# Kernel tuning notes

Measured on AMD Instinct MI355X. Metric: run time of the kernel, lower is better.

Reference implementation:

```python
import jax, jax.numpy as jnp
import numpy as np

N = 50000       # nodes
E = 1600000     # edges (avg degree 32)
IN = 128        # node_in_dim
D = 64          # node_out_dim (= GRU hidden)
H = 1           # heads
ED = 3          # edge_in_dim
STEPS = 3       # num_step_message_passing
EPS = 1e-5      # BatchNorm eps
SLOPE = 0.2     # LeakyReLU negative slope (GAT default)


def setup_inputs() -> dict:
    key = jax.random.key(0)
    ks = jax.random.split(key, 16)
    s_in = 1.0 / np.sqrt(IN)
    s_d = 1.0 / np.sqrt(D)
    return {
        "x": jax.random.normal(ks[0], (N, IN), jnp.float32),
        "edge_attr": jax.random.normal(ks[1], (E, ED), jnp.float32),
        "mlp_w": jax.random.normal(ks[2], (IN, D), jnp.float32) * s_in,
        "mlp_b": jnp.zeros((D,), jnp.float32),
        "bn_g": jnp.ones((D,), jnp.float32),
        "bn_b": jnp.zeros((D,), jnp.float32),
        "conv_w": jax.random.normal(ks[3], (D, H * D), jnp.float32) * s_d,
        "att_dst": jax.random.normal(ks[4], (H, D), jnp.float32) * s_d,
        "att_src": jax.random.normal(ks[5], (H, D), jnp.float32) * s_d,
        "att_edge": jax.random.normal(ks[6], (H, ED), jnp.float32) * s_d,
        "w_ih": jax.random.normal(ks[7], (3 * D, H * D), jnp.float32) * s_d,
        "w_hh": jax.random.normal(ks[8], (3 * D, D), jnp.float32) * s_d,
        "b_ih": jnp.zeros((3 * D,), jnp.float32),
        "b_hh": jnp.zeros((3 * D,), jnp.float32),
        "lin_w": jax.random.normal(ks[9], (IN, D), jnp.float32) * s_in,
        "lin_b": jnp.zeros((D,), jnp.float32),
        "edge_index": jax.random.randint(ks[10], (2, E), 0, N, jnp.int64),
    }


def _egat_conv(out, edge_attr, src, dst, conv_w, att_dst, att_src, att_edge):
    # out: [N, D] -> xt: [N, H, D]
    xt = (out @ conv_w).reshape(N, H, D)
    # per-node attention halves (avoid gathering twice): [N, H]
    a_dst_n = jnp.einsum("nhd,hd->nh", xt, att_dst)
    a_src_n = jnp.einsum("nhd,hd->nh", xt, att_src)
    # per-edge logits: [E, H]
    logits = a_dst_n[dst] + a_src_n[src] + edge_attr @ att_edge.T
    logits = jnp.where(logits >= 0, logits, SLOPE * logits)
    # segment softmax over destination nodes
    seg_max = jax.ops.segment_max(logits, dst, num_segments=N)  # [N, H]
    seg_max = jnp.where(jnp.isfinite(seg_max), seg_max, 0.0)
    expd = jnp.exp(logits - seg_max[dst])
    denom = jax.ops.segment_sum(expd, dst, num_segments=N)      # [N, H]
    alpha = expd / denom[dst]                                   # [E, H]
    # attention-weighted aggregation of source features
    msgs = alpha[:, :, None] * xt[src]                          # [E, H, D]
    agg = jax.ops.segment_sum(msgs, dst, num_segments=N)        # [N, H, D]
    return agg.reshape(N, H * D)


def _gru_cell(x_in, h, w_ih, w_hh, b_ih, b_hh):
    gi = x_in @ w_ih.T + b_ih
    gh = h @ w_hh.T + b_hh
    gi_r, gi_z, gi_n = jnp.split(gi, 3, axis=-1)
    gh_r, gh_z, gh_n = jnp.split(gh, 3, axis=-1)
    r = jax.nn.sigmoid(gi_r + gh_r)
    z = jax.nn.sigmoid(gi_z + gh_z)
    n = jnp.tanh(gi_n + r * gh_n)
    return (1.0 - z) * n + z * h


def reference(x, edge_attr, mlp_w, mlp_b, bn_g, bn_b, conv_w, att_dst,
              att_src, att_edge, w_ih, w_hh, b_ih, b_hh, lin_w, lin_b,
              edge_index):
    src, dst = edge_index[0], edge_index[1]
    # initial embedding: ReLU(BatchNorm(Linear(x))) with batch stats
    h0 = x @ mlp_w + mlp_b
    mu = jnp.mean(h0, axis=0)
    var = jnp.var(h0, axis=0)
    out = jax.nn.relu((h0 - mu) * jax.lax.rsqrt(var + EPS) * bn_g + bn_b)
    h = out
    for _ in range(STEPS):
        m = jax.nn.relu(_egat_conv(out, edge_attr, src, dst,
                                   conv_w, att_dst, att_src, att_edge))
        h = _gru_cell(m, h, w_ih, w_hh, b_ih, b_hh)
        out = h
    return x @ lin_w + lin_b + out
```

## Files before the change

kernel.cpp:

```cpp
#include <hip/hip_runtime.h>

typedef unsigned short ushort_t;
typedef unsigned int uint_t;
typedef __attribute__((ext_vector_type(8))) short bf16x8;
typedef __attribute__((ext_vector_type(4))) float f32x4;

#define N_NODES 50000
#define N_EDGES 1600000
#define NB_BKT 391
#define CAP_BKT 4608
#define CAP_B 6144

__device__ __forceinline__ float bfu(ushort_t u) {
    return __uint_as_float(((uint_t)u) << 16);
}
__device__ __forceinline__ ushort_t f2b(float f) {
    uint_t x = __float_as_uint(f);
    uint_t r = (x + 0x7FFFu + ((x >> 16) & 1u)) >> 16;
    return (ushort_t)r;
}
__device__ __forceinline__ float sigm(float x) {
    return 1.0f / (1.0f + __expf(-x));
}
__device__ __forceinline__ float tanh_f(float x) {
    return 1.0f - 2.0f / (__expf(2.0f * x) + 1.0f);
}
__device__ __forceinline__ bf16x8 pack8(const float* v) {
    bf16x8 r;
#pragma unroll
    for (int j = 0; j < 8; ++j) r[j] = (short)f2b(v[j]);
    return r;
}
__device__ __forceinline__ int ld_src(const int* __restrict__ ei, int i, int f64) {
    return f64 ? ei[2 * i] : ei[i];
}
__device__ __forceinline__ int ld_dst(const int* __restrict__ ei, int i, int f64) {
    return f64 ? ei[2 * N_EDGES + 2 * i] : ei[N_EDGES + i];
}
__device__ __forceinline__ bool is_f64(const int* flag) { return flag[0] > 2048; }

__global__ void k_sentinel(float* __restrict__ out, int n) {
    int i = blockIdx.x * 256 + threadIdx.x;
    if (i < n) out[i] = 100.0f;
}

__global__ void k_prep(const float* __restrict__ w_ih, const float* __restrict__ w_hh,
                       const float* __restrict__ conv_w, const float* __restrict__ mlp_w,
                       const float* __restrict__ lin_w, const int* __restrict__ ei,
                       ushort_t* __restrict__ wb, ushort_t* __restrict__ cwb,
                       ushort_t* __restrict__ mlpT, ushort_t* __restrict__ linT,
                       int* __restrict__ flag, int* __restrict__ gtail) {
    int blk = blockIdx.x;
    if (blk < 176) {
        int t = blk * 256 + threadIdx.x;
        if (t < 24576) {
            const float* w = (t < 12288) ? w_ih : w_hh;
            wb[t] = f2b(w[t < 12288 ? t : t - 12288]);
        } else if (t < 28672) {
            int r = t - 24576;
            int j = r >> 6, k = r & 63;
            cwb[j * 64 + k] = f2b(conv_w[k * 64 + j]);
        } else if (t < 36864) {
            int r = t - 28672;
            int j = r >> 7, k = r & 127;
            mlpT[j * 128 + k] = f2b(mlp_w[k * 64 + j]);
        } else if (t < 45056) {
            int r = t - 36864;
            int j = r >> 7, k = r & 127;
            linT[j * 128 + k] = f2b(lin_w[k * 64 + j]);
        }
    } else if (blk == 176) {
        __shared__ int red[256];
        int tid = threadIdx.x;
        int zeros = 0;
#pragma unroll
        for (int j = 0; j < 16; ++j) {
            int slot = (tid * 16 + j) * 2 + 1;
            if (ei[slot] == 0) zeros++;
        }
        red[tid] = zeros;
        __syncthreads();
        for (int off = 128; off; off >>= 1) {
            if (tid < off) red[tid] += red[tid + off];
            __syncthreads();
        }
        if (tid == 0) flag[0] = red[0];
    } else {
        int b = (blk - 177) * 256 + threadIdx.x;
        if (b < NB_BKT) gtail[b] = b * CAP_BKT;
    }
}

__global__ __launch_bounds__(256) void k_emb(const float* __restrict__ x,
                                             const ushort_t* __restrict__ mlpT,
                                             const float* __restrict__ mlp_b,
                                             float* __restrict__ h0, int n) {
    int lane = threadIdx.x & 63;
    int wv = threadIdx.x >> 6;
    int tile = blockIdx.x * 4 + wv;
    if (tile * 16 >= n) return;
    int nb16 = tile * 16;
    int mrow = lane & 15, q = lane >> 4;
    const float* xp = x + (nb16 + mrow) * 128 + q * 8;
    bf16x8 a[4];
#pragma unroll
    for (int kc = 0; kc < 4; ++kc) {
        float hv[8];
        const float* p = xp + kc * 32;
#pragma unroll
        for (int j = 0; j < 8; ++j) hv[j] = p[j];
        a[kc] = pack8(hv);
    }
    f32x4 acc[4];
#pragma unroll
    for (int t = 0; t < 4; ++t) acc[t] = (f32x4){0.f, 0.f, 0.f, 0.f};
#pragma unroll
    for (int kc = 0; kc < 4; ++kc) {
#pragma unroll
        for (int t = 0; t < 4; ++t) {
            bf16x8 b = *(const bf16x8*)(mlpT + (t * 16 + mrow) * 128 + kc * 32 + q * 8);
            acc[t] = __builtin_amdgcn_mfma_f32_16x16x32_bf16(a[kc], b, acc[t], 0, 0, 0);
        }
    }
#pragma unroll
    for (int t = 0; t < 4; ++t) {
        int j = t * 16 + mrow;
        float bias = mlp_b[j];
#pragma unroll
        for (int r = 0; r < 4; ++r) h0[(nb16 + q * 4 + r) * 64 + j] = acc[t][r] + bias;
    }
}

__global__ void k_stats(const float* __restrict__ h0, float* __restrict__ stats, int n) {
    __shared__ float ssum[256], ssq[256];
    int tid = threadIdx.x;
    int gid = blockIdx.x * 256 + tid;
    int col = gid & 63;
    int rg = gid >> 6;
    float s = 0.f, s2 = 0.f;
    for (int row = rg; row < n; row += 1024) {
        float v = h0[row * 64 + col];
        s += v;
        s2 += v * v;
    }
    ssum[tid] = s;
    ssq[tid] = s2;
    __syncthreads();
    if (tid < 64) {
        s = ssum[tid] + ssum[tid + 64] + ssum[tid + 128] + ssum[tid + 192];
        s2 = ssq[tid] + ssq[tid + 64] + ssq[tid + 128] + ssq[tid + 192];
        atomicAdd(&stats[tid], s);
        atomicAdd(&stats[64 + tid], s2);
    }
}

__global__ void k_bnrelu(const float* __restrict__ h0, const float* __restrict__ stats,
                         const float* __restrict__ g, const float* __restrict__ bb,
                         float* __restrict__ h, int total, float inv_n) {
    int i = blockIdx.x * 256 + threadIdx.x;
    if (i >= total) return;
    int j = i & 63;
    float mu = stats[j] * inv_n;
    float var = fmaxf(stats[64 + j] * inv_n - mu * mu, 0.f);
    float sc = rsqrtf(var + 1e-5f) * g[j];
    float sh = bb[j] - mu * sc;
    h[i] = fmaxf(h0[i] * sc + sh, 0.f);
}

__global__ __launch_bounds__(256) void k_bucket(const int* __restrict__ ei,
                                                const int* __restrict__ flag,
                                                const float* __restrict__ ea,
                                                const float* __restrict__ ae,
                                                int* __restrict__ gtail,
                                                uint2* __restrict__ bkt, int e) {
    __shared__ int cnt[NB_BKT];
    __shared__ int gbase[NB_BKT];
    for (int i = threadIdx.x; i < NB_BKT; i += 256) cnt[i] = 0;
    __syncthreads();
    int base = blockIdx.x * 4096;
    int f64 = is_f64(flag);
    float a0 = ae[0], a1 = ae[1], a2 = ae[2];
    uint_t w0[16];
    uint_t w1[16];
    int bk[16], rk[16];
#pragma unroll
    for (int j = 0; j < 16; ++j) {
        int i = base + j * 256 + threadIdx.x;
        bk[j] = -1;
        if (i < e) {
            int d = ld_dst(ei, i, f64);
            if ((uint_t)d < (uint_t)N_NODES) {
                int s = ld_src(ei, i, f64);
                if ((uint_t)s >= (uint_t)N_NODES) s = 0;
                float ed = ea[i * 3] * a0 + ea[i * 3 + 1] * a1 + ea[i * 3 + 2] * a2;
                bk[j] = d >> 7;
                w0[j] = (uint_t)s | ((uint_t)(d & 127) << 16);
                w1[j] = __float_as_uint(ed);
                rk[j] = atomicAdd(&cnt[bk[j]], 1);
            }
        }
    }
    __syncthreads();
    for (int t = threadIdx.x; t < NB_BKT; t += 256) {
        int c = cnt[t];
        gbase[t] = c ? atomicAdd(&gtail[t], c) : 0;
    }
    __syncthreads();
#pragma unroll
    for (int j = 0; j < 16; ++j) {
        if (bk[j] >= 0) {
            int pos = gbase[bk[j]] + rk[j];
            if (pos < (bk[j] + 1) * CAP_BKT) {
                uint2 p;
                p.x = w0[j];
                p.y = w1[j];
                bkt[pos] = p;
            }
        }
    }
}

__global__ __launch_bounds__(256) void k_sortb(const int* __restrict__ gtail,
                                               const uint2* __restrict__ bkt,
                                               uint2* __restrict__ pk,
                                               int* __restrict__ rs, int n) {
    __shared__ uint2 stg[CAP_B];
    __shared__ int cnt[128];
    __shared__ int sc[128];
    __shared__ int red[256];
    int b = blockIdx.x;
    int tid = threadIdx.x;
    int partial = 0;
    for (int i = tid; i < b; i += 256) partial += min(gtail[i] - i * CAP_BKT, CAP_BKT);
    red[tid] = partial;
    __syncthreads();
    for (int off = 128; off; off >>= 1) {
        if (tid < off) red[tid] += red[tid + off];
        __syncthreads();
    }
    int obase = red[0];
    int node0 = b * 128;
    int nloc = min(128, n - node0);
    int size = min(gtail[b] - b * CAP_BKT, CAP_BKT);
    const uint2* bin = bkt + b * CAP_BKT;
    for (int i = tid; i < 128; i += 256) cnt[i] = 0;
    __syncthreads();
    for (int ofs = tid; ofs < size; ofs += 256) {
        int dlow = (bin[ofs].x >> 16) & 127;
        atomicAdd(&cnt[dlow], 1);
    }
    __syncthreads();
    if (tid < 128) sc[tid] = cnt[tid];
    __syncthreads();
    for (int off = 1; off < 128; off <<= 1) {
        int add = (tid < 128 && tid >= off) ? sc[tid - off] : 0;
        __syncthreads();
        if (tid < 128) sc[tid] += add;
        __syncthreads();
    }
    if (tid < 128) sc[tid] -= cnt[tid];
    __syncthreads();
    if (tid < nloc) rs[node0 + tid] = obase + sc[tid];
    if (b == NB_BKT - 1 && tid == 0) rs[n] = obase + size;
    for (int i = tid; i < 128; i += 256) cnt[i] = 0;
    __syncthreads();
    for (int ofs = tid; ofs < size; ofs += 256) {
        uint2 p = bin[ofs];
        int dlow = (p.x >> 16) & 127;
        int r = atomicAdd(&cnt[dlow], 1);
        int pos = sc[dlow] + r;
        uint2 q;
        q.x = p.x & 0xFFFFu;
        q.y = p.y;
        if (pos < CAP_B) stg[pos] = q;
        else pk[obase + pos] = q;
    }
    __syncthreads();
    int wlim = min(size, CAP_B);
    for (int ofs = tid; ofs < wlim; ofs += 256) pk[obase + ofs] = stg[ofs];
}

__global__ __launch_bounds__(256) void k_xt(const float* __restrict__ h,
                                            const ushort_t* __restrict__ cwb,
                                            const float* __restrict__ att_dst,
                                            const float* __restrict__ att_src,
                                            ushort_t* __restrict__ xt,
                                            float* __restrict__ adst,
                                            float* __restrict__ asrc, int n) {
    int lane = threadIdx.x & 63;
    int wv = threadIdx.x >> 6;
    int tile = blockIdx.x * 4 + wv;
    if (tile * 16 >= n) return;
    int nb16 = tile * 16;
    int mrow = lane & 15, q = lane >> 4;
    bf16x8 ah[2];
    {
        const float* hp = h + (nb16 + mrow) * 64 + q * 8;
        float hv[8];
#pragma unroll
        for (int j = 0; j < 8; ++j) hv[j] = hp[j];
        ah[0] = pack8(hv);
#pragma unroll
        for (int j = 0; j < 8; ++j) hv[j] = hp[32 + j];
        ah[1] = pack8(hv);
    }
    f32x4 acc[4];
#pragma unroll
    for (int t = 0; t < 4; ++t) acc[t] = (f32x4){0.f, 0.f, 0.f, 0.f};
#pragma unroll
    for (int kh = 0; kh < 2; ++kh) {
#pragma unroll
        for (int t = 0; t < 4; ++t) {
            bf16x8 b = *(const bf16x8*)(cwb + (t * 16 + mrow) * 64 + kh * 32 + q * 8);
            acc[t] = __builtin_amdgcn_mfma_f32_16x16x32_bf16(ah[kh], b, acc[t], 0, 0, 0);
        }
    }
    float sd[4] = {0, 0, 0, 0}, ss[4] = {0, 0, 0, 0};
#pragma unroll
    for (int t = 0; t < 4; ++t) {
        int j = t * 16 + mrow;
        float ad = att_dst[j], as = att_src[j];
#pragma unroll
        for (int r = 0; r < 4; ++r) {
            float v = acc[t][r];
            xt[(nb16 + q * 4 + r) * 64 + j] = f2b(v);
            sd[r] += v * ad;
            ss[r] += v * as;
        }
    }
#pragma unroll
    for (int off = 1; off < 16; off <<= 1) {
#pragma unroll
        for (int r = 0; r < 4; ++r) {
            sd[r] += __shfl_xor(sd[r], off);
            ss[r] += __shfl_xor(ss[r], off);
        }
    }
    if (mrow == 0) {
#pragma unroll
        for (int r = 0; r < 4; ++r) {
            adst[nb16 + q * 4 + r] = sd[r];
            asrc[nb16 + q * 4 + r] = ss[r];
        }
    }
}

__global__ __launch_bounds__(256) void k_agg(const int* __restrict__ rs,
                                             const uint2* __restrict__ pk,
                                             const float* __restrict__ adst,
                                             const float* __restrict__ asrc,
                                             const ushort_t* __restrict__ xt,
                                             ushort_t* __restrict__ m, int n) {
    __shared__ float s_w[4][64];
    __shared__ int s_s[4][64];
    int lane = threadIdx.x & 63;
    int wv = threadIdx.x >> 6;
    int v = blockIdx.x * 4 + wv;
    if (v >= n) return;
    int start = rs[v], end = rs[v + 1];
    if (start >= end) {
        m[v * 64 + lane] = 0;
        return;
    }
    float adv = adst[v];
    int g = lane >> 3;
    int cb = (lane & 7) * 8;
    float acc[8] = {0, 0, 0, 0, 0, 0, 0, 0};
    float dsum = 0.f;
    for (int base = start; base < end; base += 64) {
        int e = base + lane;
        float w = 0.f;
        int s = 0;
        if (e < end) {
            uint2 p = pk[e];
            s = (int)p.x;
            float l = adv + asrc[s] + __uint_as_float(p.y);
            l = (l >= 0.f) ? l : 0.2f * l;
            w = __expf(l);
        }
        dsum += w;
        s_w[wv][lane] = w;
        s_s[wv][lane] = s;
        int cnt = min(64, end - base);
        int nb8 = (cnt + 7) >> 3;
        for (int tb = 0; tb < nb8; ++tb) {
            int sl = tb * 8 + g;
            float w8 = s_w[wv][sl];
            int s8 = s_s[wv][sl];
            uint4 qv = *(const uint4*)(xt + s8 * 64 + cb);
            acc[0] += w8 * __uint_as_float(qv.x << 16);
            acc[1] += w8 * __uint_as_float(qv.x & 0xFFFF0000u);
            acc[2] += w8 * __uint_as_float(qv.y << 16);
            acc[3] += w8 * __uint_as_float(qv.y & 0xFFFF0000u);
            acc[4] += w8 * __uint_as_float(qv.z << 16);
            acc[5] += w8 * __uint_as_float(qv.z & 0xFFFF0000u);
            acc[6] += w8 * __uint_as_float(qv.w << 16);
            acc[7] += w8 * __uint_as_float(qv.w & 0xFFFF0000u);
        }
    }
#pragma unroll
    for (int off = 32; off; off >>= 1) dsum += __shfl_xor(dsum, off);
#pragma unroll
    for (int off = 8; off < 64; off <<= 1) {
#pragma unroll
        for (int j = 0; j < 8; ++j) acc[j] += __shfl_xor(acc[j], off);
    }
    float inv = 1.0f / fmaxf(dsum, 1e-20f);
    if (g == 0) {
        uint4 o;
        o.x = (uint_t)f2b(fmaxf(acc[0] * inv, 0.f)) |
              ((uint_t)f2b(fmaxf(acc[1] * inv, 0.f)) << 16);
        o.y = (uint_t)f2b(fmaxf(acc[2] * inv, 0.f)) |
              ((uint_t)f2b(fmaxf(acc[3] * inv, 0.f)) << 16);
        o.z = (uint_t)f2b(fmaxf(acc[4] * inv, 0.f)) |
              ((uint_t)f2b(fmaxf(acc[5] * inv, 0.f)) << 16);
        o.w = (uint_t)f2b(fmaxf(acc[6] * inv, 0.f)) |
              ((uint_t)f2b(fmaxf(acc[7] * inv, 0.f)) << 16);
        *(uint4*)(m + v * 64 + cb) = o;
    }
}

__global__ __launch_bounds__(256) void k_gru(const ushort_t* __restrict__ mb,
                                             float* __restrict__ h,
                                             const ushort_t* __restrict__ wb,
                                             const float* __restrict__ b_ih,
                                             const float* __restrict__ b_hh, int n) {
    int lane = threadIdx.x & 63;
    int wv = threadIdx.x >> 6;
    int tile = blockIdx.x * 4 + wv;
    if (tile * 16 >= n) return;
    int nb16 = tile * 16;
    int mrow = lane & 15, q = lane >> 4;
    bf16x8 am[2], ah[2];
    {
        const ushort_t* mp = mb + (nb16 + mrow) * 64 + q * 8;
        am[0] = *(const bf16x8*)(mp);
        am[1] = *(const bf16x8*)(mp + 32);
        const float* hp = h + (nb16 + mrow) * 64 + q * 8;
        float hv[8];
#pragma unroll
        for (int j = 0; j < 8; ++j) hv[j] = hp[j];
        ah[0] = pack8(hv);
#pragma unroll
        for (int j = 0; j < 8; ++j) hv[j] = hp[32 + j];
        ah[1] = pack8(hv);
    }
    f32x4 acc[24];
#pragma unroll
    for (int t = 0; t < 24; ++t) acc[t] = (f32x4){0.f, 0.f, 0.f, 0.f};
#pragma unroll
    for (int kh = 0; kh < 2; ++kh) {
#pragma unroll
        for (int t = 0; t < 12; ++t) {
            bf16x8 b = *(const bf16x8*)(wb + (t * 16 + mrow) * 64 + kh * 32 + q * 8);
            acc[t] = __builtin_amdgcn_mfma_f32_16x16x32_bf16(am[kh], b, acc[t], 0, 0, 0);
        }
#pragma unroll
        for (int t = 0; t < 12; ++t) {
            bf16x8 b =
                *(const bf16x8*)(wb + (192 + t * 16 + mrow) * 64 + kh * 32 + q * 8);
            acc[12 + t] =
                __builtin_amdgcn_mfma_f32_16x16x32_bf16(ah[kh], b, acc[12 + t], 0, 0, 0);
        }
    }
#pragma unroll
    for (int t = 0; t < 4; ++t) {
        int j = t * 16 + mrow;
        float bir = b_ih[j], biz = b_ih[64 + j], bin = b_ih[128 + j];
        float bhr = b_hh[j], bhz = b_hh[64 + j], bhn = b_hh[128 + j];
#pragma unroll
        for (int r = 0; r < 4; ++r) {
            int node = nb16 + q * 4 + r;
            float gr = acc[t][r] + bir + acc[12 + t][r] + bhr;
            float gz = acc[4 + t][r] + biz + acc[16 + t][r] + bhz;
            float rr = sigm(gr);
            float zz = sigm(gz);
            float tt = acc[8 + t][r] + bin + rr * (acc[20 + t][r] + bhn);
            float hp = h[node * 64 + j];
            h[node * 64 + j] = (1.f - zz) * tanh_f(tt) + zz * hp;
        }
    }
}

__global__ __launch_bounds__(256) void k_out(const float* __restrict__ x,
                                             const ushort_t* __restrict__ linT,
                                             const float* __restrict__ lin_b,
                                             const float* __restrict__ h,
                                             float* __restrict__ out, int n) {
    int lane = threadIdx.x & 63;
    int wv = threadIdx.x >> 6;
    int tile = blockIdx.x * 4 + wv;
    if (tile * 16 >= n) return;
    int nb16 = tile * 16;
    int mrow = lane & 15, q = lane >> 4;
    const float* xp = x + (nb16 + mrow) * 128 + q * 8;
    bf16x8 a[4];
#pragma unroll
    for (int kc = 0; kc < 4; ++kc) {
        float hv[8];
        const float* p = xp + kc * 32;
#pragma unroll
        for (int j = 0; j < 8; ++j) hv[j] = p[j];
        a[kc] = pack8(hv);
    }
    f32x4 acc[4];
#pragma unroll
    for (int t = 0; t < 4; ++t) acc[t] = (f32x4){0.f, 0.f, 0.f, 0.f};
#pragma unroll
    for (int kc = 0; kc < 4; ++kc) {
#pragma unroll
        for (int t = 0; t < 4; ++t) {
            bf16x8 b = *(const bf16x8*)(linT + (t * 16 + mrow) * 128 + kc * 32 + q * 8);
            acc[t] = __builtin_amdgcn_mfma_f32_16x16x32_bf16(a[kc], b, acc[t], 0, 0, 0);
        }
    }
#pragma unroll
    for (int t = 0; t < 4; ++t) {
        int j = t * 16 + mrow;
        float bias = lin_b[j];
#pragma unroll
        for (int r = 0; r < 4; ++r) {
            int node = nb16 + q * 4 + r;
            out[node * 64 + j] = acc[t][r] + bias + h[node * 64 + j];
        }
    }
}

extern "C" void kernel_launch(void* const* d_in, const int* in_sizes, int n_in,
                              void* d_out, int out_size, void* d_ws, size_t ws_size,
                              hipStream_t stream) {
    const float* x = (const float*)d_in[0];
    const float* edge_attr = (const float*)d_in[1];
    const float* mlp_w = (const float*)d_in[2];
    const float* mlp_b = (const float*)d_in[3];
    const float* bn_g = (const float*)d_in[4];
    const float* bn_b = (const float*)d_in[5];
    const float* conv_w = (const float*)d_in[6];
    const float* att_dst = (const float*)d_in[7];
    const float* att_src = (const float*)d_in[8];
    const float* att_edge = (const float*)d_in[9];
    const float* w_ih = (const float*)d_in[10];
    const float* w_hh = (const float*)d_in[11];
    const float* b_ih = (const float*)d_in[12];
    const float* b_hh = (const float*)d_in[13];
    const float* lin_w = (const float*)d_in[14];
    const float* lin_b = (const float*)d_in[15];
    const int* ei = (const int*)d_in[16];

    char* ws = (char*)d_ws;
    float* f_h = (float*)(ws + 0);
    ushort_t* mb = (ushort_t*)(ws + 12800000);
    ushort_t* xt = (ushort_t*)(ws + 19200000);
    uint2* bkt = (uint2*)(ws + 25600000);
    uint2* pk = (uint2*)(ws + 40013824);
    float* f_adst = (float*)(ws + 52813824);
    float* f_asrc = (float*)(ws + 53014016);
    int* row_start = (int*)(ws + 53214208);
    float* stats = (float*)(ws + 53414656);
    int* flag = (int*)(ws + 53415168);
    ushort_t* wb = (ushort_t*)(ws + 53415680);
    ushort_t* cwb = (ushort_t*)(ws + 53464832);
    ushort_t* mlpT = (ushort_t*)(ws + 53473024);
    ushort_t* linT = (ushort_t*)(ws + 53489408);
    int* gtail = (int*)(ws + 53505792);

    const size_t needed = 53507840;
    if (ws_size < needed) {
        k_sentinel<<<(out_size + 255) / 256, 256, 0, stream>>>((float*)d_out, out_size);
        return;
    }

    const int n = N_NODES, e = N_EDGES;
    const int gT = ((n + 15) / 16 + 3) / 4;
    const int gN4 = (n + 3) / 4;
    const int gEl = (n * 64 + 255) / 256;
    const int gBk = (e + 4095) / 4096;
    const int gPrep = 176 + 1 + (NB_BKT + 255) / 256;

    hipMemsetAsync(stats, 0, 512, stream);

    k_prep<<<gPrep, 256, 0, stream>>>(w_ih, w_hh, conv_w, mlp_w, lin_w, ei, wb, cwb,
                                      mlpT, linT, flag, gtail);
    k_emb<<<gT, 256, 0, stream>>>(x, mlpT, mlp_b, f_h, n);
    k_stats<<<256, 256, 0, stream>>>(f_h, stats, n);
    k_bnrelu<<<gEl, 256, 0, stream>>>(f_h, stats, bn_g, bn_b, f_h, n * 64,
                                      1.0f / (float)n);

    k_bucket<<<gBk, 256, 0, stream>>>(ei, flag, edge_attr, att_edge, gtail, bkt, e);
    k_sortb<<<NB_BKT, 256, 0, stream>>>(gtail, bkt, pk, row_start, n);

    for (int s = 0; s < 3; ++s) {
        k_xt<<<gT, 256, 0, stream>>>(f_h, cwb, att_dst, att_src, xt, f_adst, f_asrc, n);
        k_agg<<<gN4, 256, 0, stream>>>(row_start, pk, f_adst, f_asrc, xt, mb, n);
        k_gru<<<gT, 256, 0, stream>>>(mb, f_h, wb, b_ih, b_hh, n);
    }

    k_out<<<gT, 256, 0, stream>>>(x, linT, lin_b, f_h, (float*)d_out, n);
}
```

Baseline: 422.9 us.

## Merge preprocessing kernels, fold BN into first xt pass, pack edges to 32-bit

Combines edge bucketing with the embedding GEMM in one launch and the bucket sort with the BN statistics reduction in another, so independent work shares a grid. The BatchNorm+ReLU pass is removed and applied inside the first k_xt iteration, which also writes the normalized h back. Sorted edge records shrink from 8 to 4 bytes by storing the edge logit term as bf16 next to a 16-bit source index. This cuts launches and memory traffic in the aggregation loop, at the cost of some precision loss in the edge attention term.

After: 403.9 us. -4.5%, faster.

```diff
diff --git a/kernel.cpp b/kernel.cpp
--- a/kernel.cpp
+++ b/kernel.cpp
@@ -10,6 +10,7 @@
 #define NB_BKT 391
 #define CAP_BKT 4608
 #define CAP_B 6144
+#define GBK 391
 
 __device__ __forceinline__ float bfu(ushort_t u) {
     return __uint_as_float(((uint_t)u) << 16);
@@ -91,202 +92,204 @@
     }
 }
 
-__global__ __launch_bounds__(256) void k_emb(const float* __restrict__ x,
-                                             const ushort_t* __restrict__ mlpT,
-                                             const float* __restrict__ mlp_b,
-                                             float* __restrict__ h0, int n) {
-    int lane = threadIdx.x & 63;
-    int wv = threadIdx.x >> 6;
-    int tile = blockIdx.x * 4 + wv;
-    if (tile * 16 >= n) return;
-    int nb16 = tile * 16;
-    int mrow = lane & 15, q = lane >> 4;
-    const float* xp = x + (nb16 + mrow) * 128 + q * 8;
-    bf16x8 a[4];
-#pragma unroll
-    for (int kc = 0; kc < 4; ++kc) {
-        float hv[8];
-        const float* p = xp + kc * 32;
-#pragma unroll
-        for (int j = 0; j < 8; ++j) hv[j] = p[j];
-        a[kc] = pack8(hv);
-    }
-    f32x4 acc[4];
-#pragma unroll
-    for (int t = 0; t < 4; ++t) acc[t] = (f32x4){0.f, 0.f, 0.f, 0.f};
-#pragma unroll
-    for (int kc = 0; kc < 4; ++kc) {
+__global__ __launch_bounds__(256) void k_embbkt(
+    const int* __restrict__ ei, const int* __restrict__ flag,
+    const float* __restrict__ ea, const float* __restrict__ ae,
+    int* __restrict__ gtail, uint2* __restrict__ bkt, int e,
+    const float* __restrict__ x, const ushort_t* __restrict__ mlpT,
+    const float* __restrict__ mlp_b, float* __restrict__ h0, int n) {
+    if (blockIdx.x < GBK) {
+        __shared__ int cnt[NB_BKT];
+        __shared__ int gbase[NB_BKT];
+        for (int i = threadIdx.x; i < NB_BKT; i += 256) cnt[i] = 0;
+        __syncthreads();
+        int base = blockIdx.x * 4096;
+        int f64 = is_f64(flag);
+        float a0 = ae[0], a1 = ae[1], a2 = ae[2];
+        uint_t w0[16], w1[16];
+        int bk[16], rk[16];
+#pragma unroll
+        for (int j = 0; j < 16; ++j) {
+            int i = base + j * 256 + threadIdx.x;
+            bk[j] = -1;
+            if (i < e) {
+                int d = ld_dst(ei, i, f64);
+                if ((uint_t)d < (uint_t)N_NODES) {
+                    int s = ld_src(ei, i, f64);
+                    if ((uint_t)s >= (uint_t)N_NODES) s = 0;
+                    float ed = ea[i * 3] * a0 + ea[i * 3 + 1] * a1 + ea[i * 3 + 2] * a2;
+                    bk[j] = d >> 7;
+                    w0[j] = (uint_t)s | ((uint_t)(d & 127) << 16);
+                    w1[j] = __float_as_uint(ed);
+                    rk[j] = atomicAdd(&cnt[bk[j]], 1);
+                }
+            }
+        }
+        __syncthreads();
+        for (int t = threadIdx.x; t < NB_BKT; t += 256) {
+            int c = cnt[t];
+            gbase[t] = c ? atomicAdd(&gtail[t], c) : 0;
+        }
+        __syncthreads();
+#pragma unroll
+        for (int j = 0; j < 16; ++j) {
+            if (bk[j] >= 0) {
+                int pos = gbase[bk[j]] + rk[j];
+                if (pos < (bk[j] + 1) * CAP_BKT) {
+                    uint2 p;
+                    p.x = w0[j];
+                    p.y = w1[j];
+                    bkt[pos] = p;
+                }
+            }
+        }
+    } else {
+        int lane = threadIdx.x & 63;
+        int wv = threadIdx.x >> 6;
+        int tile = (blockIdx.x - GBK) * 4 + wv;
+        if (tile * 16 >= n) return;
+        int nb16 = tile * 16;
+        int mrow = lane & 15, q = lane >> 4;
+        const float* xp = x + (nb16 + mrow) * 128 + q * 8;
+        bf16x8 a[4];
+#pragma unroll
+        for (int kc = 0; kc < 4; ++kc) {
+            float hv[8];
+            const float* p = xp + kc * 32;
+#pragma unroll
+            for (int j = 0; j < 8; ++j) hv[j] = p[j];
+            a[kc] = pack8(hv);
+        }
+        f32x4 acc[4];
+#pragma unroll
+        for (int t = 0; t < 4; ++t) acc[t] = (f32x4){0.f, 0.f, 0.f, 0.f};
+#pragma unroll
+        for (int kc = 0; kc < 4; ++kc) {
+#pragma unroll
+            for (int t = 0; t < 4; ++t) {
+                bf16x8 b =
+                    *(const bf16x8*)(mlpT + (t * 16 + mrow) * 128 + kc * 32 + q * 8);
+                acc[t] = __builtin_amdgcn_mfma_f32_16x16x32_bf16(a[kc], b, acc[t], 0, 0, 0);
+            }
+        }
 #pragma unroll
         for (int t = 0; t < 4; ++t) {
-            bf16x8 b = *(const bf16x8*)(mlpT + (t * 16 + mrow) * 128 + kc * 32 + q * 8);
-            acc[t] = __builtin_amdgcn_mfma_f32_16x16x32_bf16(a[kc], b, acc[t], 0, 0, 0);
-        }
-    }
-#pragma unroll
-    for (int t = 0; t < 4; ++t) {
-        int j = t * 16 + mrow;
-        float bias = mlp_b[j];
-#pragma unroll
-        for (int r = 0; r < 4; ++r) h0[(nb16 + q * 4 + r) * 64 + j] = acc[t][r] + bias;
-    }
-}
-
-__global__ void k_stats(const float* __restrict__ h0, float* __restrict__ stats, int n) {
-    __shared__ float ssum[256], ssq[256];
+            int j = t * 16 + mrow;
+            float bias = mlp_b[j];
+#pragma unroll
+            for (int r = 0; r < 4; ++r)
+                h0[(nb16 + q * 4 + r) * 64 + j] = acc[t][r] + bias;
+        }
+    }
+}
+
+__global__ __launch_bounds__(256) void k_statsort(
+    const int* __restrict__ gtail, const uint2* __restrict__ bkt,
+    uint_t* __restrict__ pk, int* __restrict__ rs, int n,
+    const float* __restrict__ h0, float* __restrict__ stats) {
+    __shared__ char smem[26624];
     int tid = threadIdx.x;
-    int gid = blockIdx.x * 256 + tid;
-    int col = gid & 63;
-    int rg = gid >> 6;
-    float s = 0.f, s2 = 0.f;
-    for (int row = rg; row < n; row += 1024) {
-        float v = h0[row * 64 + col];
-        s += v;
-        s2 += v * v;
-    }
-    ssum[tid] = s;
-    ssq[tid] = s2;
-    __syncthreads();
-    if (tid < 64) {
-        s = ssum[tid] + ssum[tid + 64] + ssum[tid + 128] + ssum[tid + 192];
-        s2 = ssq[tid] + ssq[tid + 64] + ssq[tid + 128] + ssq[tid + 192];
-        atomicAdd(&stats[tid], s);
-        atomicAdd(&stats[64 + tid], s2);
-    }
-}
-
-__global__ void k_bnrelu(const float* __restrict__ h0, const float* __restrict__ stats,
-                         const float* __restrict__ g, const float* __restrict__ bb,
-                         float* __restrict__ h, int total, float inv_n) {
-    int i = blockIdx.x * 256 + threadIdx.x;
-    if (i >= total) return;
-    int j = i & 63;
-    float mu = stats[j] * inv_n;
-    float var = fmaxf(stats[64 + j] * inv_n - mu * mu, 0.f);
-    float sc = rsqrtf(var + 1e-5f) * g[j];
-    float sh = bb[j] - mu * sc;
-    h[i] = fmaxf(h0[i] * sc + sh, 0.f);
-}
-
-__global__ __launch_bounds__(256) void k_bucket(const int* __restrict__ ei,
-                                                const int* __restrict__ flag,
-                                                const float* __restrict__ ea,
-                                                const float* __restrict__ ae,
-                                                int* __restrict__ gtail,
-                                                uint2* __restrict__ bkt, int e) {
-    __shared__ int cnt[NB_BKT];
-    __shared__ int gbase[NB_BKT];
-    for (int i = threadIdx.x; i < NB_BKT; i += 256) cnt[i] = 0;
-    __syncthreads();
-    int base = blockIdx.x * 4096;
-    int f64 = is_f64(flag);
-    float a0 = ae[0], a1 = ae[1], a2 = ae[2];
-    uint_t w0[16];
-    uint_t w1[16];
-    int bk[16], rk[16];
-#pragma unroll
-    for (int j = 0; j < 16; ++j) {
-        int i = base + j * 256 + threadIdx.x;
-        bk[j] = -1;
-        if (i < e) {
-            int d = ld_dst(ei, i, f64);
-            if ((uint_t)d < (uint_t)N_NODES) {
-                int s = ld_src(ei, i, f64);
-                if ((uint_t)s >= (uint_t)N_NODES) s = 0;
-                float ed = ea[i * 3] * a0 + ea[i * 3 + 1] * a1 + ea[i * 3 + 2] * a2;
-                bk[j] = d >> 7;
-                w0[j] = (uint_t)s | ((uint_t)(d & 127) << 16);
-                w1[j] = __float_as_uint(ed);
-                rk[j] = atomicAdd(&cnt[bk[j]], 1);
-            }
-        }
-    }
-    __syncthreads();
-    for (int t = threadIdx.x; t < NB_BKT; t += 256) {
-        int c = cnt[t];
-        gbase[t] = c ? atomicAdd(&gtail[t], c) : 0;
-    }
-    __syncthreads();
-#pragma unroll
-    for (int j = 0; j < 16; ++j) {
-        if (bk[j] >= 0) {
-            int pos = gbase[bk[j]] + rk[j];
-            if (pos < (bk[j] + 1) * CAP_BKT) {
-                uint2 p;
-                p.x = w0[j];
-                p.y = w1[j];
-                bkt[pos] = p;
-            }
-        }
-    }
-}
-
-__global__ __launch_bounds__(256) void k_sortb(const int* __restrict__ gtail,
-                                               const uint2* __restrict__ bkt,
-                                               uint2* __restrict__ pk,
-                                               int* __restrict__ rs, int n) {
-    __shared__ uint2 stg[CAP_B];
-    __shared__ int cnt[128];
-    __shared__ int sc[128];
-    __shared__ int red[256];
-    int b = blockIdx.x;
-    int tid = threadIdx.x;
-    int partial = 0;
-    for (int i = tid; i < b; i += 256) partial += min(gtail[i] - i * CAP_BKT, CAP_BKT);
-    red[tid] = partial;
-    __syncthreads();
-    for (int off = 128; off; off >>= 1) {
-        if (tid < off) red[tid] += red[tid + off];
-        __syncthreads();
-    }
-    int obase = red[0];
-    int node0 = b * 128;
-    int nloc = min(128, n - node0);
-    int size = min(gtail[b] - b * CAP_BKT, CAP_BKT);
-    const uint2* bin = bkt + b * CAP_BKT;
-    for (int i = tid; i < 128; i += 256) cnt[i] = 0;
-    __syncthreads();
-    for (int ofs = tid; ofs < size; ofs += 256) {
-        int dlow = (bin[ofs].x >> 16) & 127;
-        atomicAdd(&cnt[dlow], 1);
-    }
-    __syncthreads();
-    if (tid < 128) sc[tid] = cnt[tid];
-    __syncthreads();
-    for (int off = 1; off < 128; off <<= 1) {
-        int add = (tid < 128 && tid >= off) ? sc[tid - off] : 0;
-        __syncthreads();
-        if (tid < 128) sc[tid] += add;
-        __syncthreads();
-    }
-    if (tid < 128) sc[tid] -= cnt[tid];
-    __syncthreads();
-    if (tid < nloc) rs[node0 + tid] = obase + sc[tid];
-    if (b == NB_BKT - 1 && tid == 0) rs[n] = obase + size;
-    for (int i = tid; i < 128; i += 256) cnt[i] = 0;
-    __syncthreads();
-    for (int ofs = tid; ofs < size; ofs += 256) {
-        uint2 p = bin[ofs];
-        int dlow = (p.x >> 16) & 127;
-        int r = atomicAdd(&cnt[dlow], 1);
-        int pos = sc[dlow] + r;
-        uint2 q;
-        q.x = p.x & 0xFFFFu;
-        q.y = p.y;
-        if (pos < CAP_B) stg[pos] = q;
-        else pk[obase + pos] = q;
-    }
-    __syncthreads();
-    int wlim = min(size, CAP_B);
-    for (int ofs = tid; ofs < wlim; ofs += 256) pk[obase + ofs] = stg[ofs];
-}
-
-__global__ __launch_bounds__(256) void k_xt(const float* __restrict__ h,
+    if (blockIdx.x < NB_BKT) {
+        int* red = (int*)smem;
+        int* cnt = (int*)(smem + 1024);
+        int* sc = (int*)(smem + 1536);
+        uint_t* stg = (uint_t*)(smem + 2048);
+        int b = blockIdx.x;
+        int partial = 0;
+        for (int i = tid; i < b; i += 256)
+            partial += min(gtail[i] - i * CAP_BKT, CAP_BKT);
+        red[tid] = partial;
+        __syncthreads();
+        for (int off = 128; off; off >>= 1) {
+            if (tid < off) red[tid] += red[tid + off];
+            __syncthreads();
+        }
+        int obase = red[0];
+        int node0 = b * 128;
+        int nloc = min(128, n - node0);
+        int size = min(gtail[b] - b * CAP_BKT, CAP_BKT);
+        const uint2* bin = bkt + b * CAP_BKT;
+        for (int i = tid; i < 128; i += 256) cnt[i] = 0;
+        __syncthreads();
+        for (int ofs = tid; ofs < size; ofs += 256) {
+            int dlow = (bin[ofs].x >> 16) & 127;
+            atomicAdd(&cnt[dlow], 1);
+        }
+        __syncthreads();
+        if (tid < 128) sc[tid] = cnt[tid];
+        __syncthreads();
+        for (int off = 1; off < 128; off <<= 1) {
+            int add = (tid < 128 && tid >= off) ? sc[tid - off] : 0;
+            __syncthreads();
+            if (tid < 128) sc[tid] += add;
+            __syncthreads();
+        }
+        if (tid < 128) sc[tid] -= cnt[tid];
+        __syncthreads();
+        if (tid < nloc) rs[node0 + tid] = obase + sc[tid];
+        if (b == NB_BKT - 1 && tid == 0) rs[n] = obase + size;
+        for (int i = tid; i < 128; i += 256) cnt[i] = 0;
+        __syncthreads();
+        for (int ofs = tid; ofs < size; ofs += 256) {
+            uint2 p = bin[ofs];
+            int dlow = (p.x >> 16) & 127;
+            int r = atomicAdd(&cnt[dlow], 1);
+            int pos = sc[dlow] + r;
+            uint_t q = (p.x & 0xFFFFu) |
+                       ((uint_t)f2b(__uint_as_float(p.y)) << 16);
+            if (pos < CAP_B) stg[pos] = q;
+            else pk[obase + pos] = q;
+        }
+        __syncthreads();
+        int wlim = min(size, CAP_B);
+        for (int ofs = tid; ofs < wlim; ofs += 256) pk[obase + ofs] = stg[ofs];
+    } else {
+        float* ssum = (float*)smem;
+        float* ssq = (float*)(smem + 1024);
+        int gid = (blockIdx.x - NB_BKT) * 256 + tid;
+        int col = gid & 63;
+        int rg = gid >> 6;
+        float s = 0.f, s2 = 0.f;
+        for (int row = rg; row < n; row += 1024) {
+            float v = h0[row * 64 + col];
+            s += v;
+            s2 += v * v;
+        }
+        ssum[tid] = s;
+        ssq[tid] = s2;
+        __syncthreads();
+        if (tid < 64) {
+            s = ssum[tid] + ssum[tid + 64] + ssum[tid + 128] + ssum[tid + 192];
+            s2 = ssq[tid] + ssq[tid + 64] + ssq[tid + 128] + ssq[tid + 192];
+            atomicAdd(&stats[tid], s);
+            atomicAdd(&stats[64 + tid], s2);
+        }
+    }
+}
+
+__global__ __launch_bounds__(256) void k_xt(float* __restrict__ h,
                                             const ushort_t* __restrict__ cwb,
                                             const float* __restrict__ att_dst,
                                             const float* __restrict__ att_src,
+                                            const float* __restrict__ bn_g,
+                                            const float* __restrict__ bn_b,
+                                            const float* __restrict__ stats,
+                                            float inv_n, int apply,
                                             ushort_t* __restrict__ xt,
                                             float* __restrict__ adst,
                                             float* __restrict__ asrc, int n) {
+    __shared__ float scb[64], shb[64];
+    if (apply) {
+        int tid = threadIdx.x;
+        if (tid < 64) {
+            float mu = stats[tid] * inv_n;
+            float var = fmaxf(stats[64 + tid] * inv_n - mu * mu, 0.f);
+            float sc = rsqrtf(var + 1e-5f) * bn_g[tid];
+            scb[tid] = sc;
+            shb[tid] = bn_b[tid] - mu * sc;
+        }
+        __syncthreads();
+    }
     int lane = threadIdx.x & 63;
     int wv = threadIdx.x >> 6;
     int tile = blockIdx.x * 4 + wv;
@@ -295,14 +298,23 @@
     int mrow = lane & 15, q = lane >> 4;
     bf16x8 ah[2];
     {
-        const float* hp = h + (nb16 + mrow) * 64 + q * 8;
+        float* hp = h + (nb16 + mrow) * 64 + q * 8;
         float hv[8];
 #pragma unroll
-        for (int j = 0; j < 8; ++j) hv[j] = hp[j];
-        ah[0] = pack8(hv);
-#pragma unroll
-        for (int j = 0; j < 8; ++j) hv[j] = hp[32 + j];
-        ah[1] = pack8(hv);
+        for (int kh = 0; kh < 2; ++kh) {
+            float* p = hp + kh * 32;
+#pragma unroll
+            for (int j = 0; j < 8; ++j) hv[j] = p[j];
+            if (apply) {
+                int cb = kh * 32 + q * 8;
+#pragma unroll
+                for (int j = 0; j < 8; ++j) {
+                    hv[j] = fmaxf(hv[j] * scb[cb + j] + shb[cb + j], 0.f);
+                    p[j] = hv[j];
+                }
+            }
+            ah[kh] = pack8(hv);
+        }
     }
     f32x4 acc[4];
 #pragma unroll
@@ -346,7 +358,7 @@
 }
 
 __global__ __launch_bounds__(256) void k_agg(const int* __restrict__ rs,
-                                             const uint2* __restrict__ pk,
+                                             const uint_t* __restrict__ pk,
                                              const float* __restrict__ adst,
                                              const float* __restrict__ asrc,
                                              const ushort_t* __restrict__ xt,
@@ -372,9 +384,9 @@
         float w = 0.f;
         int s = 0;
         if (e < end) {
-            uint2 p = pk[e];
-            s = (int)p.x;
-            float l = adv + asrc[s] + __uint_as_float(p.y);
+            uint_t p = pk[e];
+            s = (int)(p & 0xFFFFu);
+            float l = adv + asrc[s] + bfu((ushort_t)(p >> 16));
             l = (l >= 0.f) ? l : 0.2f * l;
             w = __expf(l);
         }
@@ -552,19 +564,19 @@
     ushort_t* mb = (ushort_t*)(ws + 12800000);
     ushort_t* xt = (ushort_t*)(ws + 19200000);
     uint2* bkt = (uint2*)(ws + 25600000);
-    uint2* pk = (uint2*)(ws + 40013824);
-    float* f_adst = (float*)(ws + 52813824);
-    float* f_asrc = (float*)(ws + 53014016);
-    int* row_start = (int*)(ws + 53214208);
-    float* stats = (float*)(ws + 53414656);
-    int* flag = (int*)(ws + 53415168);
-    ushort_t* wb = (ushort_t*)(ws + 53415680);
-    ushort_t* cwb = (ushort_t*)(ws + 53464832);
-    ushort_t* mlpT = (ushort_t*)(ws + 53473024);
-    ushort_t* linT = (ushort_t*)(ws + 53489408);
-    int* gtail = (int*)(ws + 53505792);
-
-    const size_t needed = 53507840;
+    uint_t* pk = (uint_t*)(ws + 40013824);
+    float* f_adst = (float*)(ws + 46413824);
+    float* f_asrc = (float*)(ws + 46614016);
+    int* row_start = (int*)(ws + 46814208);
+    float* stats = (float*)(ws + 47014656);
+    int* flag = (int*)(ws + 47015168);
+    ushort_t* wb = (ushort_t*)(ws + 47015680);
+    ushort_t* cwb = (ushort_t*)(ws + 47064832);
+    ushort_t* mlpT = (ushort_t*)(ws + 47073024);
+    ushort_t* linT = (ushort_t*)(ws + 47089408);
+    int* gtail = (int*)(ws + 47105792);
+
+    const size_t needed = 47107840;
     if (ws_size < needed) {
         k_sentinel<<<(out_size + 255) / 256, 256, 0, stream>>>((float*)d_out, out_size);
         return;
@@ -573,24 +585,21 @@
     const int n = N_NODES, e = N_EDGES;
     const int gT = ((n + 15) / 16 + 3) / 4;
     const int gN4 = (n + 3) / 4;
-    const int gEl = (n * 64 + 255) / 256;
-    const int gBk = (e + 4095) / 4096;
     const int gPrep = 176 + 1 + (NB_BKT + 255) / 256;
+    const float inv_n = 1.0f / (float)n;
 
     hipMemsetAsync(stats, 0, 512, stream);
 
     k_prep<<<gPrep, 256, 0, stream>>>(w_ih, w_hh, conv_w, mlp_w, lin_w, ei, wb, cwb,
                                       mlpT, linT, flag, gtail);
-    k_emb<<<gT, 256, 0, stream>>>(x, mlpT, mlp_b, f_h, n);
-    k_stats<<<256, 256, 0, stream>>>(f_h, stats, n);
-    k_bnrelu<<<gEl, 256, 0, stream>>>(f_h, stats, bn_g, bn_b, f_h, n * 64,
-                                      1.0f / (float)n);
-
-    k_bucket<<<gBk, 256, 0, stream>>>(ei, flag, edge_attr, att_edge, gtail, bkt, e);
-    k_sortb<<<NB_BKT, 256, 0, stream>>>(gtail, bkt, pk, row_start, n);
+    k_embbkt<<<GBK + gT, 256, 0, stream>>>(ei, flag, edge_attr, att_edge, gtail, bkt, e,
+                                           x, mlpT, mlp_b, f_h, n);
+    k_statsort<<<NB_BKT + 256, 256, 0, stream>>>(gtail, bkt, pk, row_start, n, f_h,
+                                                 stats);
 
     for (int s = 0; s < 3; ++s) {
-        k_xt<<<gT, 256, 0, stream>>>(f_h, cwb, att_dst, att_src, xt, f_adst, f_asrc, n);
+        k_xt<<<gT, 256, 0, stream>>>(f_h, cwb, att_dst, att_src, bn_g, bn_b, stats,
+                                     inv_n, s == 0 ? 1 : 0, xt, f_adst, f_asrc, n);
         k_agg<<<gN4, 256, 0, stream>>>(row_start, pk, f_adst, f_asrc, xt, mb, n);
         k_gru<<<gT, 256, 0, stream>>>(mb, f_h, wb, b_ih, b_hh, n);
     }
```
